# Performance work log

Measured on AMD Instinct MI355X. Metric: run time of the kernel, lower is better.

## Reference

```python
import jax, jax.numpy as jnp
import numpy as np

DK, DV, DMODEL, HEADNUM = 64, 64, 1024, 16
SEQ = 4096


def setup_inputs() -> dict:
    key = jax.random.key(0)
    ks = jax.random.split(key, 7)
    s = 0.02
    return {
        "q": jax.random.normal(ks[0], (SEQ, DMODEL), dtype=jnp.float32),
        "k": jax.random.normal(ks[1], (SEQ, DMODEL), dtype=jnp.float32),
        "v": jax.random.normal(ks[2], (SEQ, DMODEL), dtype=jnp.float32),
        # per-head projection weights, stored batched: [H, dmodel, dk]
        "Wq": jax.random.normal(ks[3], (HEADNUM, DMODEL, DK), dtype=jnp.float32) * s,
        "Wk": jax.random.normal(ks[4], (HEADNUM, DMODEL, DK), dtype=jnp.float32) * s,
        "Wv": jax.random.normal(ks[5], (HEADNUM, DMODEL, DV), dtype=jnp.float32) * s,
        # output linear (torch Linear weight [out, in]; y = x @ W.T)
        "Wo": jax.random.normal(ks[6], (DK * HEADNUM, DK * HEADNUM), dtype=jnp.float32) * s,
    }


def reference(q, k, v, Wq, Wk, Wv, Wo):
    # batched per-head projections: [H, S, dk/dv]
    qh = jnp.einsum("sd,hdk->hsk", q, Wq)
    kh = jnp.einsum("sd,hdk->hsk", k, Wk)
    vh = jnp.einsum("sd,hdv->hsv", v, Wv)
    scale = 1.0 / jnp.sqrt(jnp.asarray(DK, dtype=qh.dtype))
    scores = jnp.einsum("hqk,hsk->hqs", qh, kh) * scale  # [H, S, S]
    attn = jax.nn.softmax(scores, axis=-1)
    heads = jnp.einsum("hqs,hsv->hqv", attn, vh)  # [H, S, dv]
    # concat heads along feature dim: [S, H*dv]
    head_cat = jnp.transpose(heads, (1, 0, 2)).reshape(SEQ, HEADNUM * DV)
    return head_cat @ Wo.T
```

## Files before the change

kernel.cpp:

```cpp
#include <hip/hip_runtime.h>

#define SEQ 4096
#define DMODEL 1024
#define HEADNUM 16
#define DHEAD 64

typedef __attribute__((ext_vector_type(8))) short short8;
typedef __attribute__((ext_vector_type(4))) float f32x4;
typedef __attribute__((ext_vector_type(16))) float f32x16;
typedef __attribute__((ext_vector_type(4))) int i32x4;

__device__ __forceinline__ short f2bf(float f) {
    unsigned u = __float_as_uint(f);
    u = (u + 0x7fffu + ((u >> 16) & 1u)) >> 16;
    return (short)u;
}

__device__ __forceinline__ float bf2f(short s) {
    return __uint_as_float(((unsigned)(unsigned short)s) << 16);
}

__device__ __forceinline__ short8 cvt8(const float4 a, const float4 b) {
    short8 r;
    r[0] = f2bf(a.x); r[1] = f2bf(a.y); r[2] = f2bf(a.z); r[3] = f2bf(a.w);
    r[4] = f2bf(b.x); r[5] = f2bf(b.y); r[6] = f2bf(b.z); r[7] = f2bf(b.w);
    return r;
}

__device__ __forceinline__ int cvtpk_bf16(float lo, float hi) {
    int r;
    asm("v_cvt_pk_bf16_f32 %0, %1, %2" : "=v"(r) : "v"(lo), "v"(hi));
    return r;
}

__device__ __forceinline__ float fexp2(float x) {
    float r;
    asm("v_exp_f32 %0, %1" : "=v"(r) : "v"(x));
    return r;
}

__device__ __forceinline__ void perml32(int& a, int& b) {
    asm("v_permlane32_swap_b32 %0, %1" : "+v"(a), "+v"(b));
}

__device__ __forceinline__ void gld16(const void* g, void* l) {
    __builtin_amdgcn_global_load_lds(
        (const __attribute__((address_space(1))) void*)g,
        (__attribute__((address_space(3))) void*)l, 16, 0, 0);
}

__global__ __launch_bounds__(256) void prep_kernel(
    const float* __restrict__ q, const float* __restrict__ k,
    const float* __restrict__ v, const float* __restrict__ Wq,
    const float* __restrict__ Wk, const float* __restrict__ Wv,
    short* __restrict__ WT, short* __restrict__ qb,
    short* __restrict__ kb, short* __restrict__ vb) {
    int bid = blockIdx.x;
    int tid = threadIdx.x;
    __shared__ short tl[64][66];
    if (bid < 768) {
        int which = bid >> 8;
        int r = bid & 255;
        int h = r >> 4;
        int d0 = (r & 15) * 64;
        const float* W = which == 0 ? Wq : (which == 1 ? Wk : Wv);
        short* dst = WT + (size_t)which * (HEADNUM * DHEAD * DMODEL);
        int c = tid & 63, r4 = tid >> 6;
#pragma unroll
        for (int i = 0; i < 16; ++i) {
            int d = i * 4 + r4;
            tl[c][d] = f2bf(W[((size_t)h * DMODEL + d0 + d) * DHEAD + c]);
        }
        __syncthreads();
#pragma unroll
        for (int i = 0; i < 16; ++i) {
            int n = i * 4 + r4;
            dst[((size_t)h * DHEAD + n) * DMODEL + d0 + c] = tl[n][c];
        }
    } else {
        int i = (bid - 768) * 256 + tid;
        int seg = i >> 19;
        int off = i & ((1 << 19) - 1);
        const float* src = seg == 0 ? q : (seg == 1 ? k : v);
        short* dst = seg == 0 ? qb : (seg == 1 ? kb : vb);
        const float4* p = (const float4*)(src + (size_t)off * 8);
        *(short8*)(dst + (size_t)off * 8) = cvt8(p[0], p[1]);
    }
}

__global__ __launch_bounds__(256) void cast_bf16_kernel(const float* __restrict__ in,
                                                        short* __restrict__ out, int n8) {
    int i = blockIdx.x * 256 + threadIdx.x;
    if (i >= n8) return;
    const float4* p = (const float4*)(in + (size_t)i * 8);
    *(short8*)(out + (size_t)i * 8) = cvt8(p[0], p[1]);
}

__device__ __forceinline__ void gemm_body(
    char* glds, const short* __restrict__ A, const short* __restrict__ Bw,
    short* __restrict__ outb, float* __restrict__ outf, int mode) {
    int b = blockIdx.x;
    int wgid = (b & 7) * 64 + (b >> 3);
    int bi = wgid >> 3;
    int ni = wgid & 7;
    int i0 = bi * 64, j0 = ni * 128;

    int tid = threadIdx.x;
    int lane = tid & 63;
    int wv = tid >> 6;
    int l15 = lane & 15;
    int g = lane >> 4;
    int wm = wv >> 1, wn = wv & 1;

    int ja0 = tid * 16, ja1 = ja0 + 4096;
    int sa0 = (ja0 >> 7) * 2048 + ((ja0 & 127) ^ (((ja0 >> 7) & 7) << 4));
    int sa1 = (ja1 >> 7) * 2048 + ((ja1 & 127) ^ (((ja1 >> 7) & 7) << 4));
    int jb0 = tid * 16, jb1 = jb0 + 4096, jb2 = jb0 + 8192, jb3 = jb0 + 12288;
    int sb0 = (jb0 >> 7) * 2048 + ((jb0 & 127) ^ (((jb0 >> 7) & 7) << 4));
    int sb1 = (jb1 >> 7) * 2048 + ((jb1 & 127) ^ (((jb1 >> 7) & 7) << 4));
    int sb2 = (jb2 >> 7) * 2048 + ((jb2 & 127) ^ (((jb2 >> 7) & 7) << 4));
    int sb3 = (jb3 >> 7) * 2048 + ((jb3 & 127) ^ (((jb3 >> 7) & 7) << 4));

    const char* Ab = (const char*)A + (size_t)i0 * 2048;
    const char* Bb = (const char*)Bw + (size_t)j0 * 2048;

#define GSTAGE(P, kt_)                          \
    {                                           \
        char* la_ = (P);                        \
        char* lb_ = (P) + 8192;                 \
        const char* As = Ab + (kt_) * 128;      \
        const char* Bs = Bb + (kt_) * 128;      \
        gld16(As + sa0, la_ + ja0);             \
        gld16(As + sa1, la_ + ja1);             \
        gld16(Bs + sb0, lb_ + jb0);             \
        gld16(Bs + sb1, lb_ + jb1);             \
        gld16(Bs + sb2, lb_ + jb2);             \
        gld16(Bs + sb3, lb_ + jb3);             \
    }

    f32x4 acc[2][4];
#pragma unroll
    for (int mm = 0; mm < 2; ++mm)
#pragma unroll
        for (int nn = 0; nn < 4; ++nn) acc[mm][nn] = (f32x4){0.f, 0.f, 0.f, 0.f};

#define GCOMPUTE(P)                                                                           \
    {                                                                                         \
        const char* la = (P);                                                                 \
        const char* lb = (P) + 8192;                                                          \
        _Pragma("unroll")                                                                     \
        for (int kc = 0; kc < 2; ++kc) {                                                      \
            short8 af[2], bf4[4];                                                             \
            _Pragma("unroll")                                                                 \
            for (int mm = 0; mm < 2; ++mm) {                                                  \
                int ra = wm * 32 + mm * 16 + l15;                                             \
                af[mm] = *(const short8*)(la + ra * 128 + ((kc * 64 + g * 16) ^ ((ra & 7) << 4))); \
            }                                                                                 \
            _Pragma("unroll")                                                                 \
            for (int nn = 0; nn < 4; ++nn) {                                                  \
                int rb = wn * 64 + nn * 16 + l15;                                             \
                bf4[nn] = *(const short8*)(lb + rb * 128 + ((kc * 64 + g * 16) ^ ((rb & 7) << 4))); \
            }                                                                                 \
            _Pragma("unroll")                                                                 \
            for (int mm = 0; mm < 2; ++mm)                                                    \
                _Pragma("unroll")                                                             \
                for (int nn = 0; nn < 4; ++nn)                                                \
                    acc[mm][nn] = __builtin_amdgcn_mfma_f32_16x16x32_bf16(af[mm], bf4[nn], acc[mm][nn], 0, 0, 0); \
        }                                                                                     \
    }

#define VMW(n) asm volatile("s_waitcnt vmcnt(" #n ")" ::: "memory")

    char* P0 = glds;
    char* P1 = glds + 24576;
    char* P2 = glds + 49152;
    GSTAGE(P0, 0);
    GSTAGE(P1, 1);
    for (int kt = 0; kt < 14; ++kt) {
        VMW(6);
        __builtin_amdgcn_s_barrier();
        GSTAGE(P2, kt + 2);
        GCOMPUTE(P0);
        char* tp = P0; P0 = P1; P1 = P2; P2 = tp;
    }
    VMW(6);
    __builtin_amdgcn_s_barrier();
    GCOMPUTE(P0);
    { char* tp = P0; P0 = P1; P1 = P2; P2 = tp; }
    VMW(0);
    __builtin_amdgcn_s_barrier();
    GCOMPUTE(P0);
#undef GSTAGE
#undef GCOMPUTE
#undef VMW

#pragma unroll
    for (int mm = 0; mm < 2; ++mm)
#pragma unroll
        for (int nn = 0; nn < 4; ++nn)
#pragma unroll
            for (int r = 0; r < 4; ++r) {
                int mg = i0 + wm * 32 + mm * 16 + 4 * g + r;
                int ng = j0 + wn * 64 + nn * 16 + l15;
                float val = acc[mm][nn][r];
                if (mode == 0)      outb[(size_t)mg * 1024 + ng] = f2bf(val);
                else if (mode == 1) outb[(size_t)ng * 4096 + mg] = f2bf(val);
                else                outf[(size_t)mg * 1024 + ng] = val;
            }
}

__global__ __launch_bounds__(256) void proj3_kernel(
    const short* __restrict__ qb, const short* __restrict__ kb,
    const short* __restrict__ vb, const short* __restrict__ WT,
    short* __restrict__ qh, short* __restrict__ kh, short* __restrict__ vt) {
    __shared__ __align__(16) char glds[3 * 24576];
    int which = blockIdx.y;
    const short* A = which == 0 ? qb : (which == 1 ? kb : vb);
    const short* B = WT + (size_t)which * (HEADNUM * DHEAD * DMODEL);
    short* outb = which == 0 ? qh : (which == 1 ? kh : vt);
    gemm_body(glds, A, B, outb, 0, which == 2 ? 1 : 0);
}

__global__ __launch_bounds__(256) void ogemm_kernel(
    const short* __restrict__ hc, const short* __restrict__ Wob,
    float* __restrict__ out) {
    __shared__ __align__(16) char glds[3 * 24576];
    gemm_body(glds, hc, Wob, 0, out, 2);
}

__global__ __launch_bounds__(256, 3) void attn_kernel(
    const short* __restrict__ qh, const short* __restrict__ kh,
    const short* __restrict__ vt, short* __restrict__ poA,
    short* __restrict__ poC, float* __restrict__ lbuf) {
    int b = blockIdx.x;
    int wg = (b & 7) * 96 + (b >> 3);
    int h = wg / 48;
    int rem = wg - h * 48;
    int split = rem >> 4;
    int qb = rem & 15;

    int tid = threadIdx.x;
    int lane = tid & 63;
    int wv = tid >> 6;
    int l31 = lane & 31;
    int hh = lane >> 5;
    int qbase = qb * 256 + wv * 64;
    int kv0 = split * 1376;
    int nt = (split < 2) ? 43 : 42;

    short* pob = (split < 2) ? poA + (size_t)split * SEQ * DMODEL : poC;

    __shared__ __align__(16) char lds_all[3 * 8192];

    const short* qpA = qh + (size_t)(qbase + l31) * 1024 + h * 64 + hh * 8;
    const short* qpB = qpA + 32 * 1024;
    short8 bqA0 = *(const short8*)(qpA);
    short8 bqA1 = *(const short8*)(qpA + 16);
    short8 bqA2 = *(const short8*)(qpA + 32);
    short8 bqA3 = *(const short8*)(qpA + 48);
    short8 bqB0 = *(const short8*)(qpB);
    short8 bqB1 = *(const short8*)(qpB + 16);
    short8 bqB2 = *(const short8*)(qpB + 32);
    short8 bqB3 = *(const short8*)(qpB + 48);

    const char* kbaseh = (const char*)kh + h * 128;
    const char* vbaseh = (const char*)vt + (size_t)h * 64 * 8192;

    int krow = tid >> 3;
    int kcol = (tid & 7) * 16;
    int ksrc = krow * 2048 + (kcol ^ ((krow & 7) << 4));
    int vrow = tid >> 2;
    int vswc = ((tid & 3) * 16) ^ (((vrow >> 1) & 3) << 4);
    size_t vsrcb = (size_t)vrow * 8192 + vswc;
    int ldst = tid * 16;

#define STAGE(P, kvg) {                                            \
    gld16(kbaseh + (size_t)(kvg) * 2048 + ksrc, (P) + ldst);       \
    gld16(vbaseh + (size_t)(kvg) * 2 + vsrcb, (P) + 4096 + ldst); }

    float lsumA = 0.f, lsumB = 0.f;
    f32x16 oaA0 = {}, oaA1 = {}, oaB0 = {}, oaB1 = {};

    int ksw = (l31 & 7) << 4;
    int hh16 = hh * 16;
    int vswz = (l31 >> 1) & 3;
    const float C1 = 0.18033688f;
    const float MB_ = 5.77078016f;

    char* p0 = lds_all;
    char* p1 = lds_all + 8192;
    char* p2 = lds_all + 16384;

    STAGE(p0, kv0);
    STAGE(p1, kv0 + 32);

#define VMW(n) asm volatile("s_waitcnt vmcnt(" #n ")" ::: "memory")

#define SOFTMAX(S, LSUM, PC0, PC1) {                                           \
    float e_[16];                                                              \
    _Pragma("unroll")                                                          \
    for (int i_ = 0; i_ < 16; ++i_) e_[i_] = fexp2(fmaf((S)[i_], C1, -MB_));   \
    LSUM += ((e_[0]+e_[1])+(e_[2]+e_[3])) + ((e_[4]+e_[5])+(e_[6]+e_[7]))      \
          + ((e_[8]+e_[9])+(e_[10]+e_[11])) + ((e_[12]+e_[13])+(e_[14]+e_[15])); \
    int pk0 = cvtpk_bf16(e_[0], e_[1]),   pk1 = cvtpk_bf16(e_[2], e_[3]);      \
    int pk2 = cvtpk_bf16(e_[4], e_[5]),   pk3 = cvtpk_bf16(e_[6], e_[7]);      \
    int pk4 = cvtpk_bf16(e_[8], e_[9]),   pk5 = cvtpk_bf16(e_[10], e_[11]);    \
    int pk6 = cvtpk_bf16(e_[12], e_[13]), pk7 = cvtpk_bf16(e_[14], e_[15]);    \
    perml32(pk0, pk2); perml32(pk1, pk3);                                      \
    perml32(pk4, pk6); perml32(pk5, pk7);                                      \
    i32x4 v0_; v0_[0] = pk0; v0_[1] = pk1; v0_[2] = pk2; v0_[3] = pk3;         \
    i32x4 v1_; v1_[0] = pk4; v1_[1] = pk5; v1_[2] = pk6; v1_[3] = pk7;         \
    PC0 = *(short8*)&v0_;                                                      \
    PC1 = *(short8*)&v1_; }

#define COMPUTE(KP) {                                                          \
    const char* kp_ = (KP);                                                    \
    const char* vp_ = (KP) + 4096;                                             \
    short8 ak0 = *(const short8*)(kp_ + l31 * 128 + ((0   + hh16) ^ ksw));     \
    short8 ak1 = *(const short8*)(kp_ + l31 * 128 + ((32  + hh16) ^ ksw));     \
    short8 ak2 = *(const short8*)(kp_ + l31 * 128 + ((64  + hh16) ^ ksw));     \
    short8 ak3 = *(const short8*)(kp_ + l31 * 128 + ((96  + hh16) ^ ksw));     \
    f32x16 sA = {}, sB = {};                                                   \
    __builtin_amdgcn_s_setprio(1);                                             \
    sA = __builtin_amdgcn_mfma_f32_32x32x16_bf16(ak0, bqA0, sA, 0, 0, 0);      \
    sA = __builtin_amdgcn_mfma_f32_32x32x16_bf16(ak1, bqA1, sA, 0, 0, 0);      \
    sA = __builtin_amdgcn_mfma_f32_32x32x16_bf16(ak2, bqA2, sA, 0, 0, 0);      \
    sA = __builtin_amdgcn_mfma_f32_32x32x16_bf16(ak3, bqA3, sA, 0, 0, 0);      \
    sB = __builtin_amdgcn_mfma_f32_32x32x16_bf16(ak0, bqB0, sB, 0, 0, 0);      \
    sB = __builtin_amdgcn_mfma_f32_32x32x16_bf16(ak1, bqB1, sB, 0, 0, 0);      \
    sB = __builtin_amdgcn_mfma_f32_32x32x16_bf16(ak2, bqB2, sB, 0, 0, 0);      \
    sB = __builtin_amdgcn_mfma_f32_32x32x16_bf16(ak3, bqB3, sB, 0, 0, 0);      \
    __builtin_amdgcn_s_setprio(0);                                             \
    short8 pcA0, pcA1, pcB0, pcB1;                                             \
    SOFTMAX(sA, lsumA, pcA0, pcA1);                                            \
    SOFTMAX(sB, lsumB, pcB0, pcB1);                                            \
    short8 av00 = *(const short8*)(vp_ + l31 * 64 + (((0 + hh) ^ vswz) << 4)); \
    short8 av01 = *(const short8*)(vp_ + l31 * 64 + (((2 + hh) ^ vswz) << 4)); \
    short8 av10 = *(const short8*)(vp_ + (32 + l31) * 64 + (((0 + hh) ^ vswz) << 4)); \
    short8 av11 = *(const short8*)(vp_ + (32 + l31) * 64 + (((2 + hh) ^ vswz) << 4)); \
    __builtin_amdgcn_s_setprio(1);                                             \
    oaA0 = __builtin_amdgcn_mfma_f32_32x32x16_bf16(av00, pcA0, oaA0, 0, 0, 0); \
    oaA0 = __builtin_amdgcn_mfma_f32_32x32x16_bf16(av01, pcA1, oaA0, 0, 0, 0); \
    oaA1 = __builtin_amdgcn_mfma_f32_32x32x16_bf16(av10, pcA0, oaA1, 0, 0, 0); \
    oaA1 = __builtin_amdgcn_mfma_f32_32x32x16_bf16(av11, pcA1, oaA1, 0, 0, 0); \
    oaB0 = __builtin_amdgcn_mfma_f32_32x32x16_bf16(av00, pcB0, oaB0, 0, 0, 0); \
    oaB0 = __builtin_amdgcn_mfma_f32_32x32x16_bf16(av01, pcB1, oaB0, 0, 0, 0); \
    oaB1 = __builtin_amdgcn_mfma_f32_32x32x16_bf16(av10, pcB0, oaB1, 0, 0, 0); \
    oaB1 = __builtin_amdgcn_mfma_f32_32x32x16_bf16(av11, pcB1, oaB1, 0, 0, 0); \
    __builtin_amdgcn_s_setprio(0); }

    for (int t = 0; t < nt - 2; ++t) {
        VMW(2);
        __builtin_amdgcn_s_barrier();
        STAGE(p2, kv0 + (t + 2) * 32);
        COMPUTE(p0);
        char* tp = p0; p0 = p1; p1 = p2; p2 = tp;
    }
    VMW(2);
    __builtin_amdgcn_s_barrier();
    COMPUTE(p0);
    { char* tp = p0; p0 = p1; p1 = p2; p2 = tp; }
    VMW(0);
    __builtin_amdgcn_s_barrier();
    COMPUTE(p0);
#undef COMPUTE
#undef SOFTMAX
#undef STAGE
#undef VMW

    {
        float ltA = lsumA + __shfl_xor(lsumA, 32);
        int qA = qbase + l31;
        if (hh == 0) lbuf[(size_t)(split * 16 + h) * 4096 + qA] = ltA;
        short* pr = pob + (size_t)qA * 1024 + h * 64 + hh * 4;
#pragma unroll
        for (int rp = 0; rp < 8; ++rp) {
            int dvb = ((2 * rp) & 3) + 8 * (rp >> 1);
            *(int*)(pr + dvb) = cvtpk_bf16(oaA0[2 * rp], oaA0[2 * rp + 1]);
            *(int*)(pr + 32 + dvb) = cvtpk_bf16(oaA1[2 * rp], oaA1[2 * rp + 1]);
        }
    }
    {
        float ltB = lsumB + __shfl_xor(lsumB, 32);
        int qB = qbase + 32 + l31;
        if (hh == 0) lbuf[(size_t)(split * 16 + h) * 4096 + qB] = ltB;
        short* pr = pob + (size_t)qB * 1024 + h * 64 + hh * 4;
#pragma unroll
        for (int rp = 0; rp < 8; ++rp) {
            int dvb = ((2 * rp) & 3) + 8 * (rp >> 1);
            *(int*)(pr + dvb) = cvtpk_bf16(oaB0[2 * rp], oaB0[2 * rp + 1]);
            *(int*)(pr + 32 + dvb) = cvtpk_bf16(oaB1[2 * rp], oaB1[2 * rp + 1]);
        }
    }
}

__global__ __launch_bounds__(256) void attn_reduce_kernel(
    const short* __restrict__ poA, const short* __restrict__ poC,
    const float* __restrict__ lbuf, short* __restrict__ hc) {
    int idx = blockIdx.x * 256 + threadIdx.x;
    int q = idx >> 7;
    int cb = (idx & 127) * 8;
    int h = cb >> 6;
    float l = lbuf[(size_t)h * 4096 + q] + lbuf[(size_t)(16 + h) * 4096 + q] +
              lbuf[(size_t)(32 + h) * 4096 + q];
    float inv = 1.f / l;
    short8 a = *(const short8*)(poA + (size_t)q * 1024 + cb);
    short8 b2 = *(const short8*)(poA + (size_t)(4096 + q) * 1024 + cb);
    short8 c = *(const short8*)(poC + (size_t)q * 1024 + cb);
    short8 r;
#pragma unroll
    for (int j = 0; j < 8; ++j)
        r[j] = f2bf((bf2f(a[j]) + bf2f(b2[j]) + bf2f(c[j])) * inv);
    *(short8*)(hc + (size_t)q * 1024 + cb) = r;
}

extern "C" void kernel_launch(void* const* d_in, const int* in_sizes, int n_in,
                              void* d_out, int out_size, void* d_ws, size_t ws_size,
                              hipStream_t stream) {
    const float* q  = (const float*)d_in[0];
    const float* k  = (const float*)d_in[1];
    const float* v  = (const float*)d_in[2];
    const float* Wq = (const float*)d_in[3];
    const float* Wk = (const float*)d_in[4];
    const float* Wv = (const float*)d_in[5];
    const float* Wo = (const float*)d_in[6];
    float* out = (float*)d_out;

    char* ws = (char*)d_ws;
    const size_t MB = 1u << 20;
    short* WqT  = (short*)(ws + 0 * MB);
    short* qh   = (short*)(ws + 6 * MB);
    short* kh   = (short*)(ws + 14 * MB);
    short* vt   = (short*)(ws + 22 * MB);
    short* qbws = (short*)(ws + 30 * MB);
    float* lbuf = (float*)(ws + 38 * MB);
    short* Wob  = WqT;
    short* kb = (short*)d_out;
    short* vb = (short*)d_out + SEQ * DMODEL;
    short* poA = (short*)d_out;
    short* poC = qbws;
    short* hc = qh;

    prep_kernel<<<dim3(768 + 6144), 256, 0, stream>>>(
        q, k, v, Wq, Wk, Wv, WqT, qbws, kb, vb);

    proj3_kernel<<<dim3(512, 3), 256, 0, stream>>>(qbws, kb, vb, WqT, qh, kh, vt);

    int n8w = DMODEL * DMODEL / 8;
    cast_bf16_kernel<<<dim3(n8w / 256), 256, 0, stream>>>(Wo, Wob, n8w);

    attn_kernel<<<dim3(768), 256, 0, stream>>>(qh, kh, vt, poA, poC, lbuf);

    attn_reduce_kernel<<<dim3(2048), 256, 0, stream>>>(poA, poC, lbuf, hc);

    ogemm_kernel<<<dim3(512), 256, 0, stream>>>(hc, Wob, out);
}
```

Baseline: 170.8 us.

## Fuse fp32-to-bf16 input cast into projection GEMM A-tile loads

The projection GEMM now reads fp32 q/k/v directly into registers, converts them to bf16, and writes them into the swizzled LDS tile, with a three-buffer pipeline. This removes the separate cast pass and its write and re-read of the bf16 activations. The Wo cast is folded into the attention-reduce launch to save a kernel launch. In exchange the A tiles go through registers instead of direct global-to-LDS loads, each A load moves twice the bytes, and the pipeline has to wait on vmcnt(0) every iteration.

```diff
diff --git a/kernel.cpp b/kernel.cpp
--- a/kernel.cpp
+++ b/kernel.cpp
@@ -49,56 +49,32 @@
         (__attribute__((address_space(3))) void*)l, 16, 0, 0);
 }
 
-__global__ __launch_bounds__(256) void prep_kernel(
-    const float* __restrict__ q, const float* __restrict__ k,
-    const float* __restrict__ v, const float* __restrict__ Wq,
-    const float* __restrict__ Wk, const float* __restrict__ Wv,
-    short* __restrict__ WT, short* __restrict__ qb,
-    short* __restrict__ kb, short* __restrict__ vb) {
-    int bid = blockIdx.x;
+__global__ __launch_bounds__(256) void wtrans_kernel(
+    const float* __restrict__ Wq, const float* __restrict__ Wk,
+    const float* __restrict__ Wv, short* __restrict__ WT) {
+    int which = blockIdx.z;
+    const float* W = which == 0 ? Wq : (which == 1 ? Wk : Wv);
+    short* dst = WT + (size_t)which * (HEADNUM * DHEAD * DMODEL);
+    int h = blockIdx.y, d0 = blockIdx.x * 64;
     int tid = threadIdx.x;
+    int c = tid & 63, r4 = tid >> 6;
     __shared__ short tl[64][66];
-    if (bid < 768) {
-        int which = bid >> 8;
-        int r = bid & 255;
-        int h = r >> 4;
-        int d0 = (r & 15) * 64;
-        const float* W = which == 0 ? Wq : (which == 1 ? Wk : Wv);
-        short* dst = WT + (size_t)which * (HEADNUM * DHEAD * DMODEL);
-        int c = tid & 63, r4 = tid >> 6;
-#pragma unroll
-        for (int i = 0; i < 16; ++i) {
-            int d = i * 4 + r4;
-            tl[c][d] = f2bf(W[((size_t)h * DMODEL + d0 + d) * DHEAD + c]);
-        }
-        __syncthreads();
-#pragma unroll
-        for (int i = 0; i < 16; ++i) {
-            int n = i * 4 + r4;
-            dst[((size_t)h * DHEAD + n) * DMODEL + d0 + c] = tl[n][c];
-        }
-    } else {
-        int i = (bid - 768) * 256 + tid;
-        int seg = i >> 19;
-        int off = i & ((1 << 19) - 1);
-        const float* src = seg == 0 ? q : (seg == 1 ? k : v);
-        short* dst = seg == 0 ? qb : (seg == 1 ? kb : vb);
-        const float4* p = (const float4*)(src + (size_t)off * 8);
-        *(short8*)(dst + (size_t)off * 8) = cvt8(p[0], p[1]);
-    }
-}
-
-__global__ __launch_bounds__(256) void cast_bf16_kernel(const float* __restrict__ in,
-                                                        short* __restrict__ out, int n8) {
-    int i = blockIdx.x * 256 + threadIdx.x;
-    if (i >= n8) return;
-    const float4* p = (const float4*)(in + (size_t)i * 8);
-    *(short8*)(out + (size_t)i * 8) = cvt8(p[0], p[1]);
-}
-
-__device__ __forceinline__ void gemm_body(
-    char* glds, const short* __restrict__ A, const short* __restrict__ Bw,
-    short* __restrict__ outb, float* __restrict__ outf, int mode) {
+#pragma unroll
+    for (int i = 0; i < 16; ++i) {
+        int d = i * 4 + r4;
+        tl[c][d] = f2bf(W[((size_t)h * DMODEL + d0 + d) * DHEAD + c]);
+    }
+    __syncthreads();
+#pragma unroll
+    for (int i = 0; i < 16; ++i) {
+        int n = i * 4 + r4;
+        dst[((size_t)h * DHEAD + n) * DMODEL + d0 + c] = tl[n][c];
+    }
+}
+
+__device__ __forceinline__ void gemm_body_f32a(
+    char* glds, const float* __restrict__ A, const short* __restrict__ Bw,
+    short* __restrict__ outb, int mode) {
     int b = blockIdx.x;
     int wgid = (b & 7) * 64 + (b >> 3);
     int bi = wgid >> 3;
@@ -112,31 +88,40 @@
     int g = lane >> 4;
     int wm = wv >> 1, wn = wv & 1;
 
-    int ja0 = tid * 16, ja1 = ja0 + 4096;
-    int sa0 = (ja0 >> 7) * 2048 + ((ja0 & 127) ^ (((ja0 >> 7) & 7) << 4));
-    int sa1 = (ja1 >> 7) * 2048 + ((ja1 & 127) ^ (((ja1 >> 7) & 7) << 4));
     int jb0 = tid * 16, jb1 = jb0 + 4096, jb2 = jb0 + 8192, jb3 = jb0 + 12288;
     int sb0 = (jb0 >> 7) * 2048 + ((jb0 & 127) ^ (((jb0 >> 7) & 7) << 4));
     int sb1 = (jb1 >> 7) * 2048 + ((jb1 & 127) ^ (((jb1 >> 7) & 7) << 4));
     int sb2 = (jb2 >> 7) * 2048 + ((jb2 & 127) ^ (((jb2 >> 7) & 7) << 4));
     int sb3 = (jb3 >> 7) * 2048 + ((jb3 & 127) ^ (((jb3 >> 7) & 7) << 4));
-
-    const char* Ab = (const char*)A + (size_t)i0 * 2048;
     const char* Bb = (const char*)Bw + (size_t)j0 * 2048;
 
-#define GSTAGE(P, kt_)                          \
-    {                                           \
-        char* la_ = (P);                        \
-        char* lb_ = (P) + 8192;                 \
-        const char* As = Ab + (kt_) * 128;      \
-        const char* Bs = Bb + (kt_) * 128;      \
-        gld16(As + sa0, la_ + ja0);             \
-        gld16(As + sa1, la_ + ja1);             \
-        gld16(Bs + sb0, lb_ + jb0);             \
-        gld16(Bs + sb1, lb_ + jb1);             \
-        gld16(Bs + sb2, lb_ + jb2);             \
-        gld16(Bs + sb3, lb_ + jb3);             \
-    }
+    int ja0 = tid * 16, ja1 = ja0 + 4096;
+    int ra0 = ja0 >> 7, ca0 = ja0 & 127;
+    int ra1 = ja1 >> 7, ca1 = ja1 & 127;
+    int da0 = ra0 * 128 + (ca0 ^ ((ra0 & 7) << 4));
+    int da1 = ra1 * 128 + (ca1 ^ ((ra1 & 7) << 4));
+    const float* As0 = A + (size_t)(i0 + ra0) * 1024 + (ca0 >> 1);
+    const float* As1 = A + (size_t)(i0 + ra1) * 1024 + (ca1 >> 1);
+
+    float4 ar00, ar01, ar10, ar11;
+
+#define AISSUE(kt_) {                                 \
+    const float* p0_ = As0 + (kt_) * 64;              \
+    const float* p1_ = As1 + (kt_) * 64;              \
+    ar00 = *(const float4*)(p0_);                     \
+    ar01 = *(const float4*)(p0_ + 4);                 \
+    ar10 = *(const float4*)(p1_);                     \
+    ar11 = *(const float4*)(p1_ + 4); }
+#define BISSUE(P, kt_) {                              \
+    char* lb_ = (P) + 8192;                           \
+    const char* Bs = Bb + (kt_) * 128;                \
+    gld16(Bs + sb0, lb_ + jb0);                       \
+    gld16(Bs + sb1, lb_ + jb1);                       \
+    gld16(Bs + sb2, lb_ + jb2);                       \
+    gld16(Bs + sb3, lb_ + jb3); }
+#define AWRITE(P) {                                   \
+    *(short8*)((P) + da0) = cvt8(ar00, ar01);         \
+    *(short8*)((P) + da1) = cvt8(ar10, ar11); }
 
     f32x4 acc[2][4];
 #pragma unroll
@@ -169,6 +154,118 @@
         }                                                                                     \
     }
 
+    char* P0 = glds;
+    char* P1 = glds + 24576;
+    char* P2 = glds + 49152;
+
+    AISSUE(0); BISSUE(P0, 0);
+    asm volatile("s_waitcnt vmcnt(0)" ::: "memory");
+    AWRITE(P0);
+    AISSUE(1); BISSUE(P1, 1);
+    for (int kt = 0; kt < 15; ++kt) {
+        asm volatile("s_waitcnt lgkmcnt(0)" ::: "memory");
+        __builtin_amdgcn_s_barrier();
+        asm volatile("s_waitcnt vmcnt(0)" ::: "memory");
+        AWRITE(P1);
+        if (kt < 14) { AISSUE(kt + 2); BISSUE(P2, kt + 2); }
+        GCOMPUTE(P0);
+        char* tp = P0; P0 = P1; P1 = P2; P2 = tp;
+    }
+    asm volatile("s_waitcnt lgkmcnt(0)" ::: "memory");
+    __builtin_amdgcn_s_barrier();
+    GCOMPUTE(P0);
+#undef AISSUE
+#undef BISSUE
+#undef AWRITE
+#undef GCOMPUTE
+
+#pragma unroll
+    for (int mm = 0; mm < 2; ++mm)
+#pragma unroll
+        for (int nn = 0; nn < 4; ++nn)
+#pragma unroll
+            for (int r = 0; r < 4; ++r) {
+                int mg = i0 + wm * 32 + mm * 16 + 4 * g + r;
+                int ng = j0 + wn * 64 + nn * 16 + l15;
+                float val = acc[mm][nn][r];
+                if (mode == 0) outb[(size_t)mg * 1024 + ng] = f2bf(val);
+                else           outb[(size_t)ng * 4096 + mg] = f2bf(val);
+            }
+}
+
+__device__ __forceinline__ void gemm_body(
+    char* glds, const short* __restrict__ A, const short* __restrict__ Bw,
+    float* __restrict__ outf) {
+    int b = blockIdx.x;
+    int wgid = (b & 7) * 64 + (b >> 3);
+    int bi = wgid >> 3;
+    int ni = wgid & 7;
+    int i0 = bi * 64, j0 = ni * 128;
+
+    int tid = threadIdx.x;
+    int lane = tid & 63;
+    int wv = tid >> 6;
+    int l15 = lane & 15;
+    int g = lane >> 4;
+    int wm = wv >> 1, wn = wv & 1;
+
+    int ja0 = tid * 16, ja1 = ja0 + 4096;
+    int sa0 = (ja0 >> 7) * 2048 + ((ja0 & 127) ^ (((ja0 >> 7) & 7) << 4));
+    int sa1 = (ja1 >> 7) * 2048 + ((ja1 & 127) ^ (((ja1 >> 7) & 7) << 4));
+    int jb0 = tid * 16, jb1 = jb0 + 4096, jb2 = jb0 + 8192, jb3 = jb0 + 12288;
+    int sb0 = (jb0 >> 7) * 2048 + ((jb0 & 127) ^ (((jb0 >> 7) & 7) << 4));
+    int sb1 = (jb1 >> 7) * 2048 + ((jb1 & 127) ^ (((jb1 >> 7) & 7) << 4));
+    int sb2 = (jb2 >> 7) * 2048 + ((jb2 & 127) ^ (((jb2 >> 7) & 7) << 4));
+    int sb3 = (jb3 >> 7) * 2048 + ((jb3 & 127) ^ (((jb3 >> 7) & 7) << 4));
+
+    const char* Ab = (const char*)A + (size_t)i0 * 2048;
+    const char* Bb = (const char*)Bw + (size_t)j0 * 2048;
+
+#define GSTAGE(P, kt_)                          \
+    {                                           \
+        char* la_ = (P);                        \
+        char* lb_ = (P) + 8192;                 \
+        const char* As = Ab + (kt_) * 128;      \
+        const char* Bs = Bb + (kt_) * 128;      \
+        gld16(As + sa0, la_ + ja0);             \
+        gld16(As + sa1, la_ + ja1);             \
+        gld16(Bs + sb0, lb_ + jb0);             \
+        gld16(Bs + sb1, lb_ + jb1);             \
+        gld16(Bs + sb2, lb_ + jb2);             \
+        gld16(Bs + sb3, lb_ + jb3);             \
+    }
+
+    f32x4 acc[2][4];
+#pragma unroll
+    for (int mm = 0; mm < 2; ++mm)
+#pragma unroll
+        for (int nn = 0; nn < 4; ++nn) acc[mm][nn] = (f32x4){0.f, 0.f, 0.f, 0.f};
+
+#define GCOMPUTE(P)                                                                           \
+    {                                                                                         \
+        const char* la = (P);                                                                 \
+        const char* lb = (P) + 8192;                                                          \
+        _Pragma("unroll")                                                                     \
+        for (int kc = 0; kc < 2; ++kc) {                                                      \
+            short8 af[2], bf4[4];                                                             \
+            _Pragma("unroll")                                                                 \
+            for (int mm = 0; mm < 2; ++mm) {                                                  \
+                int ra = wm * 32 + mm * 16 + l15;                                             \
+                af[mm] = *(const short8*)(la + ra * 128 + ((kc * 64 + g * 16) ^ ((ra & 7) << 4))); \
+            }                                                                                 \
+            _Pragma("unroll")                                                                 \
+            for (int nn = 0; nn < 4; ++nn) {                                                  \
+                int rb = wn * 64 + nn * 16 + l15;                                             \
+                bf4[nn] = *(const short8*)(lb + rb * 128 + ((kc * 64 + g * 16) ^ ((rb & 7) << 4))); \
+            }                                                                                 \
+            _Pragma("unroll")                                                                 \
+            for (int mm = 0; mm < 2; ++mm)                                                    \
+                _Pragma("unroll")                                                             \
+                for (int nn = 0; nn < 4; ++nn)                                                \
+                    acc[mm][nn] = __builtin_amdgcn_mfma_f32_16x16x32_bf16(af[mm], bf4[nn], acc[mm][nn], 0, 0, 0); \
+        }                                                                                     \
+    }
+
 #define VMW(n) asm volatile("s_waitcnt vmcnt(" #n ")" ::: "memory")
 
     char* P0 = glds;
@@ -202,30 +299,27 @@
             for (int r = 0; r < 4; ++r) {
                 int mg = i0 + wm * 32 + mm * 16 + 4 * g + r;
                 int ng = j0 + wn * 64 + nn * 16 + l15;
-                float val = acc[mm][nn][r];
-                if (mode == 0)      outb[(size_t)mg * 1024 + ng] = f2bf(val);
-                else if (mode == 1) outb[(size_t)ng * 4096 + mg] = f2bf(val);
-                else                outf[(size_t)mg * 1024 + ng] = val;
+                outf[(size_t)mg * 1024 + ng] = acc[mm][nn][r];
             }
 }
 
 __global__ __launch_bounds__(256) void proj3_kernel(
-    const short* __restrict__ qb, const short* __restrict__ kb,
-    const short* __restrict__ vb, const short* __restrict__ WT,
+    const float* __restrict__ q, const float* __restrict__ k,
+    const float* __restrict__ v, const short* __restrict__ WT,
     short* __restrict__ qh, short* __restrict__ kh, short* __restrict__ vt) {
     __shared__ __align__(16) char glds[3 * 24576];
     int which = blockIdx.y;
-    const short* A = which == 0 ? qb : (which == 1 ? kb : vb);
+    const float* A = which == 0 ? q : (which == 1 ? k : v);
     const short* B = WT + (size_t)which * (HEADNUM * DHEAD * DMODEL);
     short* outb = which == 0 ? qh : (which == 1 ? kh : vt);
-    gemm_body(glds, A, B, outb, 0, which == 2 ? 1 : 0);
+    gemm_body_f32a(glds, A, B, outb, which == 2 ? 1 : 0);
 }
 
 __global__ __launch_bounds__(256) void ogemm_kernel(
     const short* __restrict__ hc, const short* __restrict__ Wob,
     float* __restrict__ out) {
     __shared__ __align__(16) char glds[3 * 24576];
-    gemm_body(glds, hc, Wob, 0, out, 2);
+    gemm_body(glds, hc, Wob, out);
 }
 
 __global__ __launch_bounds__(256, 3) void attn_kernel(
@@ -396,8 +490,17 @@
 
 __global__ __launch_bounds__(256) void attn_reduce_kernel(
     const short* __restrict__ poA, const short* __restrict__ poC,
-    const float* __restrict__ lbuf, short* __restrict__ hc) {
-    int idx = blockIdx.x * 256 + threadIdx.x;
+    const float* __restrict__ lbuf, short* __restrict__ hc,
+    const float* __restrict__ Wo, short* __restrict__ Wob) {
+    int bid = blockIdx.x;
+    int tid = threadIdx.x;
+    if (bid >= 2048) {
+        int i = (bid - 2048) * 256 + tid;
+        const float4* p = (const float4*)(Wo + (size_t)i * 8);
+        *(short8*)(Wob + (size_t)i * 8) = cvt8(p[0], p[1]);
+        return;
+    }
+    int idx = bid * 256 + tid;
     int q = idx >> 7;
     int cb = (idx & 127) * 8;
     int h = cb >> 6;
@@ -428,30 +531,23 @@
 
     char* ws = (char*)d_ws;
     const size_t MB = 1u << 20;
-    short* WqT  = (short*)(ws + 0 * MB);
+    short* WT   = (short*)(ws + 0 * MB);
     short* qh   = (short*)(ws + 6 * MB);
     short* kh   = (short*)(ws + 14 * MB);
     short* vt   = (short*)(ws + 22 * MB);
-    short* qbws = (short*)(ws + 30 * MB);
+    short* poC  = (short*)(ws + 30 * MB);
     float* lbuf = (float*)(ws + 38 * MB);
-    short* Wob  = WqT;
-    short* kb = (short*)d_out;
-    short* vb = (short*)d_out + SEQ * DMODEL;
-    short* poA = (short*)d_out;
-    short* poC = qbws;
-    short* hc = qh;
-
-    prep_kernel<<<dim3(768 + 6144), 256, 0, stream>>>(
-        q, k, v, Wq, Wk, Wv, WqT, qbws, kb, vb);
-
-    proj3_kernel<<<dim3(512, 3), 256, 0, stream>>>(qbws, kb, vb, WqT, qh, kh, vt);
-
-    int n8w = DMODEL * DMODEL / 8;
-    cast_bf16_kernel<<<dim3(n8w / 256), 256, 0, stream>>>(Wo, Wob, n8w);
+    short* Wob  = WT;
+    short* poA  = (short*)d_out;
+    short* hc   = qh;
+
+    wtrans_kernel<<<dim3(DMODEL / 64, HEADNUM, 3), 256, 0, stream>>>(Wq, Wk, Wv, WT);
+
+    proj3_kernel<<<dim3(512, 3), 256, 0, stream>>>(q, k, v, WT, qh, kh, vt);
 
     attn_kernel<<<dim3(768), 256, 0, stream>>>(qh, kh, vt, poA, poC, lbuf);
 
-    attn_reduce_kernel<<<dim3(2048), 256, 0, stream>>>(poA, poC, lbuf, hc);
+    attn_reduce_kernel<<<dim3(2560), 256, 0, stream>>>(poA, poC, lbuf, hc, Wo, Wob);
 
     ogemm_kernel<<<dim3(512), 256, 0, stream>>>(hc, Wob, out);
 }
```

Measured after the change: 177.1 us. 3.7% more time.
